# Kernel optimization log

Hardware: AMD Instinct MI355X
Metric: run time of the kernel (lower is better)

## Reference

```python
import jax, jax.numpy as jnp
import numpy as np

EPS = 1e-5


def mish(x):
    return x * jnp.tanh(jax.nn.softplus(x))


def layer_norm(x, g, b):
    mu = jnp.mean(x, axis=-1, keepdims=True)
    var = jnp.var(x, axis=-1, keepdims=True)
    return (x - mu) / jnp.sqrt(var + EPS) * g + b


def setup_inputs() -> dict:
    key = jax.random.key(0)
    ks = jax.random.split(key, 10)
    D = 256      # hidden_size == encoder feature dim
    L = 64       # max_length
    B, N, K, Q = 2, 10, 1, 5
    NQ = N * Q   # na_rate = 0
    s = 0.02
    inp = {
        "support": jax.random.normal(ks[0], (B * N * K, L, D), jnp.float32),
        "query": jax.random.normal(ks[1], (B * NQ, L, D), jnp.float32),
        "ln_g": jnp.ones((D,), jnp.float32),
        "ln_b": jnp.zeros((D,), jnp.float32),
        "ln2_g": jnp.ones((2 * D,), jnp.float32),
        "ln2_b": jnp.zeros((2 * D,), jnp.float32),
        "proj_W": jax.random.normal(ks[2], (D, 4 * D), jnp.float32) * s,
        "proj_b": jnp.zeros((D,), jnp.float32),
        "W1": jax.random.normal(ks[3], (D, 4 * D), jnp.float32) * s,
        "b1": jnp.zeros((D,), jnp.float32),
        "W2": jax.random.normal(ks[4], (1, D), jnp.float32) * s,
        "b2": jnp.zeros((1,), jnp.float32),
        "W3": jax.random.normal(ks[5], (1, 1), jnp.float32) * s,  # MLP_out Linear(K=1, 1)
        "b3": jnp.zeros((1,), jnp.float32),
        "N": N, "K": K, "Q": Q,
    }
    return inp


def reference(support, query, ln_g, ln_b, ln2_g, ln2_b, proj_W, proj_b,
              W1, b1, W2, b2, W3, b3, N, K, Q):
    L, D = support.shape[-2], support.shape[-1]
    B = support.shape[0] // (N * K)
    NQ = query.shape[0] // B  # = N*Q + na*Q

    s = layer_norm(support, ln_g, ln_b)
    q = layer_norm(query, ln_g, ln_b)

    # expand to all (query, support) pairs: [B, NQ, N*K, L, D] -> [M, L, D]
    s_e = jnp.broadcast_to(s.reshape(B, 1, N * K, L, D), (B, NQ, N * K, L, D)).reshape(-1, L, D)
    q_e = jnp.broadcast_to(q.reshape(B, NQ, 1, L, D), (B, NQ, N * K, L, D)).reshape(-1, L, D)

    # bidirectional cross-attention (no scaling, as in the original)
    att = jnp.einsum('mld,mkd->mlk', s_e, q_e)            # [M, Ls, Lq]
    s_att = jnp.einsum('mlk,mkd->mld', jax.nn.softmax(att, axis=2), q_e)
    q_att = jnp.einsum('mlk,mld->mkd', jax.nn.softmax(att, axis=1), s_e)

    enh_s = jnp.concatenate([s_e, s_att, jnp.abs(s_e - s_att), s_e * s_att], axis=-1)
    enh_q = jnp.concatenate([q_e, q_att, jnp.abs(q_e - q_att), q_e * q_att], axis=-1)
    s_p = mish(enh_s @ proj_W.T + proj_b)
    q_p = mish(enh_q @ proj_W.T + proj_b)

    # pool_norm: max+mean over length, then LayerNorm(2D)
    s_pool = layer_norm(jnp.concatenate([jnp.max(s_p, axis=-2), jnp.mean(s_p, axis=-2)], axis=-1), ln2_g, ln2_b)
    q_pool = layer_norm(jnp.concatenate([jnp.max(q_p, axis=-2), jnp.mean(q_p, axis=-2)], axis=-1), ln2_g, ln2_b)

    cat_seq = jnp.concatenate([q_pool, s_pool], axis=-1)  # [M, 4D]
    h = mish(cat_seq @ W1.T + b1) @ W2.T + b2             # MLProc -> [M, 1]
    logits = mish(h) @ W3.T + b3                          # MLP_out (K=1) -> [M, 1]

    logits = logits.reshape(B, NQ, N)
    minn = jnp.min(logits, axis=-1)
    logits = jnp.concatenate([logits, minn[..., None] - 1.0], axis=2)  # [B, NQ, N+1]
    pred = jnp.argmax(logits.reshape(-1, N + 1), axis=1)
    return logits, pred
```

## Files before the change

### kernel.cpp

```cpp
#include <hip/hip_runtime.h>

typedef unsigned int u32;
typedef unsigned short u16;
#define LN_EPS 1e-5f

typedef __attribute__((ext_vector_type(8))) short short8v;
typedef __attribute__((ext_vector_type(4))) float f32x4;

#define MFMA(acc, a, b) acc = __builtin_amdgcn_mfma_f32_16x16x32_bf16(a, b, acc, 0, 0, 0)

__device__ __forceinline__ float wave_sum(float v){
  #pragma unroll
  for (int o = 32; o > 0; o >>= 1) v += __shfl_xor(v, o, 64);
  return v;
}
__device__ __forceinline__ float mishf(float v){
  float t = __expf(v);
  float u = t*t + 2.f*t;
  return v * (1.f - 2.f/(u + 2.f));
}
__device__ __forceinline__ float bf2f(u16 h){
  return __uint_as_float(((u32)h) << 16);
}
__device__ __forceinline__ u32 pack_split(float x){
  u32 u = __float_as_uint(x);
  u32 h = (u + 0x8000u) & 0xffff0000u;
  float lf = x - __uint_as_float(h);
  return h | (__float_as_uint(lf) >> 16);
}
__device__ __forceinline__ void split_pair(float x0, float x1, u32& hw, u32& lw){
  u32 u0 = __float_as_uint(x0), u1 = __float_as_uint(x1);
  u32 h0 = (u0 + 0x8000u) & 0xffff0000u;
  u32 h1 = (u1 + 0x8000u) & 0xffff0000u;
  float l0 = x0 - __uint_as_float(h0);
  float l1 = x1 - __uint_as_float(h1);
  hw = (h0 >> 16) | h1;
  lw = (__float_as_uint(l0) >> 16) | (__float_as_uint(l1) & 0xffff0000u);
}
__device__ __forceinline__ void split8v(f32x4 a, f32x4 b, short8v& hi, short8v& lo){
  union { short8v v; u32 w[4]; } H, L;
  split_pair(a[0], a[1], H.w[0], L.w[0]);
  split_pair(a[2], a[3], H.w[1], L.w[1]);
  split_pair(b[0], b[1], H.w[2], L.w[2]);
  split_pair(b[2], b[3], H.w[3], L.w[3]);
  hi = H.v; lo = L.v;
}
__device__ __forceinline__ void unpack8(uint4 q0, uint4 q1, short8v& hi, short8v& lo){
  union { short8v v; u32 w[4]; } H, L;
  H.w[0] = (q0.x >> 16) | (q0.y & 0xffff0000u);
  L.w[0] = (q0.x & 0xffffu) | (q0.y << 16);
  H.w[1] = (q0.z >> 16) | (q0.w & 0xffff0000u);
  L.w[1] = (q0.z & 0xffffu) | (q0.w << 16);
  H.w[2] = (q1.x >> 16) | (q1.y & 0xffff0000u);
  L.w[2] = (q1.x & 0xffffu) | (q1.y << 16);
  H.w[3] = (q1.z >> 16) | (q1.w & 0xffff0000u);
  L.w[3] = (q1.z & 0xffffu) | (q1.w << 16);
  hi = H.v; lo = L.v;
}

__global__ void k_setup_A(const float* __restrict__ sup, const float* __restrict__ qry,
                          const float* __restrict__ lng, const float* __restrict__ lnb,
                          const float* __restrict__ Wg,  const float* __restrict__ W1,
                          u16* __restrict__ SHI, u16* __restrict__ SLO,
                          u16* __restrict__ QHI, u16* __restrict__ QLO,
                          u16* __restrict__ WHI, u16* __restrict__ WLO,
                          float* __restrict__ W1T2)
{
  const int bid = blockIdx.x, t = threadIdx.x;

  if (bid < 120){
    const int seq = bid;
    const float* src; u16 *dh, *dl;
    if (seq < 20){
      src = sup + (size_t)seq*16384;
      dh = SHI + (size_t)seq*16384; dl = SLO + (size_t)seq*16384;
    } else {
      src = qry + (size_t)(seq-20)*16384;
      dh = QHI + (size_t)(seq-20)*16384; dl = QLO + (size_t)(seq-20)*16384;
    }
    const int w = t >> 6, lane = t & 63;
    float4 g4 = *(const float4*)(lng + lane*4);
    float4 b4 = *(const float4*)(lnb + lane*4);
    for (int r = w; r < 64; r += 4){
      float4 x = *(const float4*)(src + r*256 + lane*4);
      float s  = wave_sum(x.x + x.y + x.z + x.w);
      float sq = wave_sum(x.x*x.x + x.y*x.y + x.z*x.z + x.w*x.w);
      float mu = s*(1.f/256.f);
      float rstd = 1.f/sqrtf(sq*(1.f/256.f) - mu*mu + LN_EPS);
      float y0 = (x.x - mu)*rstd*g4.x + b4.x;
      float y1 = (x.y - mu)*rstd*g4.y + b4.y;
      float y2 = (x.z - mu)*rstd*g4.z + b4.z;
      float y3 = (x.w - mu)*rstd*g4.w + b4.w;
      u32 p0 = pack_split(y0), p1 = pack_split(y1), p2 = pack_split(y2), p3 = pack_split(y3);
      ushort4 hv = make_ushort4((u16)(p0>>16),(u16)(p1>>16),(u16)(p2>>16),(u16)(p3>>16));
      ushort4 lv = make_ushort4((u16)(p0&0xffffu),(u16)(p1&0xffffu),(u16)(p2&0xffffu),(u16)(p3&0xffffu));
      *(ushort4*)(dh + r*256 + lane*4) = hv;
      *(ushort4*)(dl + r*256 + lane*4) = lv;
    }
  } else if (bid < 248){
    const int gid = (bid-120)*256 + t;
    const int ks = gid >> 10, rem = gid & 1023, nt = rem >> 6, l = rem & 63;
    const int n  = nt*16 + (l & 15);
    const int k0 = ks*32 + (l >> 4)*8;
    const float* src = Wg + n*1024 + k0;
    float4 xa = *(const float4*)src;
    float4 xb = *(const float4*)(src + 4);
    f32x4 fa, fb;
    fa[0]=xa.x; fa[1]=xa.y; fa[2]=xa.z; fa[3]=xa.w;
    fb[0]=xb.x; fb[1]=xb.y; fb[2]=xb.z; fb[3]=xb.w;
    short8v hi, lo;
    split8v(fa, fb, hi, lo);
    *(short8v*)(WHI + (size_t)gid*8) = hi;
    *(short8v*)(WLO + (size_t)gid*8) = lo;
  } else {
    const int gid = (bid-248)*256 + t;
    const int kb = gid >> 8, n = gid & 255;
    float4 v = *(const float4*)(W1 + n*1024 + kb*4);
    *(float4*)(W1T2 + kb*1024 + n*4) = v;
  }
}

__global__ __launch_bounds__(256) void k_setup_xp(
    const u16* __restrict__ SHI, const u16* __restrict__ SLO,
    const u16* __restrict__ QHI, const u16* __restrict__ QLO,
    const u16* __restrict__ WHI, const u16* __restrict__ WLO,
    float* __restrict__ XPS, float* __restrict__ XPQ)
{
  const int seq = blockIdx.x;
  const u16 *Xh, *Xl; float* out;
  if (seq < 20){
    Xh = SHI + (size_t)seq*16384; Xl = SLO + (size_t)seq*16384;
    out = XPS + (size_t)seq*16384;
  } else {
    Xh = QHI + (size_t)(seq-20)*16384; Xl = QLO + (size_t)(seq-20)*16384;
    out = XPQ + (size_t)(seq-20)*16384;
  }
  const int t = threadIdx.x, w = t >> 6, l = t & 63;
  const int l15 = l & 15, l4 = l >> 4;
  const int Mg = w >> 1, Ng = w & 1;

  f32x4 acc[2][8];
  #pragma unroll
  for (int i = 0; i < 2; i++)
    #pragma unroll
    for (int j = 0; j < 8; j++){ acc[i][j][0]=0.f; acc[i][j][1]=0.f; acc[i][j][2]=0.f; acc[i][j][3]=0.f; }

  for (int ks = 0; ks < 8; ks++){
    short8v ah[2], al[2];
    #pragma unroll
    for (int mt = 0; mt < 2; mt++){
      const int ro = (Mg*32 + mt*16 + l15)*256 + ks*32 + l4*8;
      ah[mt] = *(const short8v*)(Xh + ro);
      al[mt] = *(const short8v*)(Xl + ro);
    }
    #pragma unroll
    for (int nt = 0; nt < 8; nt++){
      const int fo = (ks*16 + Ng*8 + nt)*512 + l*8;
      short8v bh = *(const short8v*)(WHI + fo);
      short8v bl = *(const short8v*)(WLO + fo);
      #pragma unroll
      for (int mt = 0; mt < 2; mt++){
        MFMA(acc[mt][nt], ah[mt], bh);
        MFMA(acc[mt][nt], ah[mt], bl);
        MFMA(acc[mt][nt], al[mt], bh);
      }
    }
  }
  #pragma unroll
  for (int mt = 0; mt < 2; mt++)
    #pragma unroll
    for (int nt = 0; nt < 8; nt++)
      #pragma unroll
      for (int r = 0; r < 4; r++)
        out[(Mg*32 + mt*16 + l4*4 + r)*256 + Ng*128 + nt*16 + l15] = acc[mt][nt][r];
}

#define WLH(BUF, C, H) { const int base_ = (((C)*8 + ch)*16 + Ng*8 + (H)*4)*512 + l*8; \
  _Pragma("unroll") for (int j_ = 0; j_ < 4; j_++){ \
    BUF[j_*2]   = *(const short8v*)(WHI + base_ + j_*512); \
    BUF[j_*2+1] = *(const short8v*)(WLO + base_ + j_*512); } }
#define WMH(BUF, G, H) { _Pragma("unroll") for (int j_ = 0; j_ < 4; j_++){ \
  MFMA(acc[0][(H)*4+j_], fh[G][0], BUF[j_*2]); \
  MFMA(acc[0][(H)*4+j_], fh[G][0], BUF[j_*2+1]); \
  MFMA(acc[0][(H)*4+j_], fl[G][0], BUF[j_*2]); \
  MFMA(acc[1][(H)*4+j_], fh[G][1], BUF[j_*2]); \
  MFMA(acc[1][(H)*4+j_], fh[G][1], BUF[j_*2+1]); \
  MFMA(acc[1][(H)*4+j_], fl[G][1], BUF[j_*2]); } }

__global__ __launch_bounds__(256, 2) void k_pair15(
    const u16* __restrict__ SHI, const u16* __restrict__ SLO,
    const u16* __restrict__ QHI, const u16* __restrict__ QLO,
    const u16* __restrict__ WHI, const u16* __restrict__ WLO,
    const float* __restrict__ XPS, const float* __restrict__ XPQ,
    const float* __restrict__ W1T2,
    const float* __restrict__ pbias,
    const float* __restrict__ ln2g, const float* __restrict__ ln2b,
    const float* __restrict__ b1,
    const float* __restrict__ W2,  const float* __restrict__ b2,
    const float* __restrict__ W3,  const float* __restrict__ b3,
    float* __restrict__ logits)
{
  __shared__ float SM[19600];
  float* S0  = SM;
  u16*   OcT = (u16*)(SM + 4352);
  float* AOc = SM + 9472;
  u32*   P   = (u32*)(SM + 14080);
  float* cat = SM + 18432;
  float* smx = SM + 19456;
  float* smi = SM + 19520;
  float* red = SM + 19584;
  float* stat= SM + 19592;
  float* mred= SM + 19594;

  const int m = (blockIdx.x & 7)*125 + (blockIdx.x >> 3);
  const int b = m / 500, rr = m % 500, nq = rr / 10, n_ = rr % 10;
  const u16* Sh = SHI + (size_t)(b*10 + n_) * 16384;
  const u16* Sl = SLO + (size_t)(b*10 + n_) * 16384;
  const u16* Qh = QHI + (size_t)(b*50 + nq) * 16384;
  const u16* Ql = QLO + (size_t)(b*50 + nq) * 16384;
  const float* xpS = XPS + (size_t)(b*10 + n_) * 16384;
  const float* xpQ = XPQ + (size_t)(b*50 + nq) * 16384;

  const int t = threadIdx.x, w = t >> 6, l = t & 63;
  const int l15 = l & 15, l4 = l >> 4;

  {
    f32x4 acc4[4];
    #pragma unroll
    for (int i = 0; i < 4; i++){ acc4[i][0]=0.f; acc4[i][1]=0.f; acc4[i][2]=0.f; acc4[i][3]=0.f; }
    const u16* Sa = Sh + (w*16+l15)*256 + l4*8;
    const u16* Sb = Sl + (w*16+l15)*256 + l4*8;
    short8v ah = *(const short8v*)Sa;
    short8v al = *(const short8v*)Sb;
    short8v bh[4], bl[4];
    #pragma unroll
    for (int nt = 0; nt < 4; nt++){
      bh[nt] = *(const short8v*)(Qh + (nt*16+l15)*256 + l4*8);
      bl[nt] = *(const short8v*)(Ql + (nt*16+l15)*256 + l4*8);
    }
    #pragma unroll
    for (int ch = 0; ch < 8; ch++){
      short8v nah, nal, nbh[4], nbl[4];
      if (ch < 7){
        nah = *(const short8v*)(Sa + (ch+1)*32);
        nal = *(const short8v*)(Sb + (ch+1)*32);
        #pragma unroll
        for (int nt = 0; nt < 4; nt++){
          nbh[nt] = *(const short8v*)(Qh + (nt*16+l15)*256 + (ch+1)*32 + l4*8);
          nbl[nt] = *(const short8v*)(Ql + (nt*16+l15)*256 + (ch+1)*32 + l4*8);
        }
      }
      #pragma unroll
      for (int nt = 0; nt < 4; nt++){
        MFMA(acc4[nt], ah, bh[nt]);
        MFMA(acc4[nt], ah, bl[nt]);
        MFMA(acc4[nt], al, bh[nt]);
      }
      if (ch < 7){
        ah = nah; al = nal;
        #pragma unroll
        for (int nt = 0; nt < 4; nt++){ bh[nt] = nbh[nt]; bl[nt] = nbl[nt]; }
      }
    }
    #pragma unroll
    for (int nt = 0; nt < 4; nt++)
      #pragma unroll
      for (int r = 0; r < 4; r++)
        S0[(w*16 + l4*4 + r)*68 + nt*16 + l15] = acc4[nt][r];
    __syncthreads();
  }

  auto softmax_row = [&](){
    if (t < 64){
      float mxv = -1e30f, sm = 0.f;
      for (int k = 0; k < 64; k++) mxv = fmaxf(mxv, S0[t*68 + k]);
      for (int k = 0; k < 64; k++) sm += __expf(S0[t*68 + k] - mxv);
      smx[t] = mxv; smi[t] = 1.f/sm;
    }
    __syncthreads();
    #pragma unroll
    for (int r = 0; r < 16; r++){
      int idx = t + 256*r, ll = idx >> 6, k = idx & 63;
      P[ll*68 + k] = pack_split(__expf(S0[ll*68 + k] - smx[ll]) * smi[ll]);
    }
    __syncthreads();
  };
  auto softmax_col_T = [&](){
    if (t < 64){
      float mxv = -1e30f, sm = 0.f;
      for (int ld = 0; ld < 64; ld++) mxv = fmaxf(mxv, S0[ld*68 + t]);
      for (int ld = 0; ld < 64; ld++) sm += __expf(S0[ld*68 + t] - mxv);
      smx[t] = mxv; smi[t] = 1.f/sm;
    }
    __syncthreads();
    #pragma unroll
    for (int r = 0; r < 16; r++){
      int idx = t + 256*r, ll = idx >> 6, k = idx & 63;
      P[k*68 + ll] = pack_split(__expf(S0[ll*68 + k] - smx[k]) * smi[k]);
    }
    __syncthreads();
  };

  auto do_side = [&](const u16* Xh, const u16* Xl, const u16* Oh, const u16* Ol,
                     const float* xp, int cat_off){
    const int Mg = w >> 1, Ng = w & 1;
    f32x4 acc[2][8];
    #pragma unroll
    for (int mt = 0; mt < 2; mt++)
      #pragma unroll
      for (int nt = 0; nt < 8; nt++){
        const float* xr = xp + (Mg*32 + mt*16 + l4*4)*256 + Ng*128 + nt*16 + l15;
        acc[mt][nt][0] = xr[0];
        acc[mt][nt][1] = xr[256];
        acc[mt][nt][2] = xr[512];
        acc[mt][nt][3] = xr[768];
      }

    short8v svh = *(const short8v*)(Oh + l*256 + w*8);
    short8v svl = *(const short8v*)(Ol + l*256 + w*8);
    #pragma unroll
    for (int e = 0; e < 8; e++){
      OcT[(w*8+e)*80 + l]        = (u16)svh[e];
      OcT[2560 + (w*8+e)*80 + l] = (u16)svl[e];
    }
    svh = *(const short8v*)(Oh + l*256 + 32 + w*8);
    svl = *(const short8v*)(Ol + l*256 + 32 + w*8);
    __syncthreads();

    const int xoff = (Mg*32 + l15)*256 + l4*8;

    #pragma unroll 1
    for (int ch = 0; ch < 8; ch++){
      short8v xh0 = *(const short8v*)(Xh + xoff + ch*32);
      short8v xl0 = *(const short8v*)(Xl + xoff + ch*32);
      short8v xh1 = *(const short8v*)(Xh + xoff + 4096 + ch*32);
      short8v xl1 = *(const short8v*)(Xl + xoff + 4096 + ch*32);
      short8v wa[8], wb[8];
      WLH(wa, 1, 0);

      {
        const u16* Ob = OcT + (ch&1)*5120;
        f32x4 ao0 = {0.f,0.f,0.f,0.f}, ao1 = {0.f,0.f,0.f,0.f};
        #pragma unroll
        for (int ks = 0; ks < 2; ks++){
          const u32* pp = P + (w*16 + l15)*68 + ks*32 + l4*8;
          uint4 q0 = *(const uint4*)pp;
          uint4 q1 = *(const uint4*)(pp + 4);
          short8v ph, pl; unpack8(q0, q1, ph, pl);
          const u16* ob0 = Ob + l15*80 + ks*32 + l4*8;
          const u16* ob1 = Ob + (16 + l15)*80 + ks*32 + l4*8;
          short8v bh0 = *(const short8v*)ob0;
          short8v bl0 = *(const short8v*)(ob0 + 2560);
          short8v bh1 = *(const short8v*)ob1;
          short8v bl1 = *(const short8v*)(ob1 + 2560);
          MFMA(ao0, ph, bh0); MFMA(ao0, ph, bl0); MFMA(ao0, pl, bh0);
          MFMA(ao1, ph, bh1); MFMA(ao1, ph, bl1); MFMA(ao1, pl, bh1);
        }
        float* Ad = AOc + (ch&1)*2304;
        #pragma unroll
        for (int r = 0; r < 4; r++){
          Ad[(w*16 + l4*4 + r)*36 + l15]      = ao0[r];
          Ad[(w*16 + l4*4 + r)*36 + 16 + l15] = ao1[r];
        }
      }

      if (ch < 7){
        u16* Ob1 = OcT + ((ch+1)&1)*5120;
        #pragma unroll
        for (int e = 0; e < 8; e++){
          Ob1[(w*8+e)*80 + l]        = (u16)svh[e];
          Ob1[2560 + (w*8+e)*80 + l] = (u16)svl[e];
        }
      }
      if (ch < 6){
        svh = *(const short8v*)(Oh + l*256 + (ch+2)*32 + w*8);
        svl = *(const short8v*)(Ol + l*256 + (ch+2)*32 + w*8);
      }
      __syncthreads();

      short8v fh[3][2], fl[3][2];
      {
        const float* Ad = AOc + (ch&1)*2304;
        f32x4 xv0[2], xv1[2], av0[2], av1[2];
        #pragma unroll
        for (int mt_ = 0; mt_ < 2; mt_++){
          short8v xh = mt_ ? xh1 : xh0;
          short8v xl = mt_ ? xl1 : xl0;
          #pragma unroll
          for (int e_ = 0; e_ < 4; e_++){
            xv0[mt_][e_] = bf2f((u16)xh[e_])     + bf2f((u16)xl[e_]);
            xv1[mt_][e_] = bf2f((u16)xh[4 + e_]) + bf2f((u16)xl[4 + e_]);
          }
          const int row = Mg*32 + mt_*16 + l15;
          av0[mt_] = *(const f32x4*)(Ad + row*36 + l4*8);
          av1[mt_] = *(const f32x4*)(Ad + row*36 + l4*8 + 4);
        }
        #pragma unroll
        for (int mt_ = 0; mt_ < 2; mt_++){
          split8v(av0[mt_], av1[mt_], fh[0][mt_], fl[0][mt_]);
          f32x4 d0, d1, p0, p1;
          #pragma unroll
          for (int e_ = 0; e_ < 4; e_++){
            d0[e_] = fabsf(xv0[mt_][e_] - av0[mt_][e_]);
            d1[e_] = fabsf(xv1[mt_][e_] - av1[mt_][e_]);
            p0[e_] = xv0[mt_][e_] * av0[mt_][e_];
            p1[e_] = xv1[mt_][e_] * av1[mt_][e_];
          }
          split8v(d0, d1, fh[1][mt_], fl[1][mt_]);
          split8v(p0, p1, fh[2][mt_], fl[2][mt_]);
        }
      }

      WLH(wb, 1, 1);
      WMH(wa, 0, 0);
      WLH(wa, 2, 0);
      WMH(wb, 0, 1);
      WLH(wb, 2, 1);
      WMH(wa, 1, 0);
      WLH(wa, 3, 0);
      WMH(wb, 1, 1);
      WLH(wb, 3, 1);
      WMH(wa, 2, 0);
      WMH(wb, 2, 1);
    }

    float* pmax2 = (float*)P;
    float* psum2 = pmax2 + 512;
    #pragma unroll
    for (int nt = 0; nt < 8; nt++){
      const int col = Ng*128 + nt*16 + l15;
      const float pb = pbias[col];
      float mx = -1e30f, sm = 0.f;
      #pragma unroll
      for (int mt_ = 0; mt_ < 2; mt_++)
        #pragma unroll
        for (int r = 0; r < 4; r++){
          float v = mishf(acc[mt_][nt][r] + pb);
          mx = fmaxf(mx, v); sm += v;
        }
      mx = fmaxf(mx, __shfl_xor(mx, 16, 64));
      mx = fmaxf(mx, __shfl_xor(mx, 32, 64));
      sm += __shfl_xor(sm, 16, 64);
      sm += __shfl_xor(sm, 32, 64);
      if (l4 == 0){ pmax2[Mg*256 + col] = mx; psum2[Mg*256 + col] = sm; }
    }
    __syncthreads();
    float v1 = fmaxf(pmax2[t], pmax2[256 + t]);
    float v2 = (psum2[t] + psum2[256 + t]) * (1.f/64.f);
    float p1 = wave_sum(v1 + v2);
    float p2 = wave_sum(v1*v1 + v2*v2);
    if (l == 0){ red[w] = p1; red[4 + w] = p2; }
    __syncthreads();
    if (t == 0){
      float s1 = red[0]+red[1]+red[2]+red[3];
      float s2 = red[4]+red[5]+red[6]+red[7];
      float mu  = s1 * (1.f/512.f);
      float var = s2 * (1.f/512.f) - mu*mu;
      stat[0] = mu; stat[1] = 1.f/sqrtf(var + LN_EPS);
    }
    __syncthreads();
    float mu = stat[0], rstd = stat[1];
    cat[cat_off + t]       = (v1 - mu)*rstd*ln2g[t]       + ln2b[t];
    cat[cat_off + 256 + t] = (v2 - mu)*rstd*ln2g[256 + t] + ln2b[256 + t];
    __syncthreads();
  };

  softmax_row();
  do_side(Sh, Sl, Qh, Ql, xpS, 512);
  softmax_col_T();
  do_side(Qh, Ql, Sh, Sl, xpQ, 0);

  {
    float acc1 = 0.f;
    const float* wt = W1T2 + t*4;
    #pragma unroll 8
    for (int kb = 0; kb < 256; kb++){
      float4 wv = *(const float4*)(wt + kb*1024);
      const float* cp = &cat[kb*4];
      acc1 += cp[0]*wv.x + cp[1]*wv.y + cp[2]*wv.z + cp[3]*wv.w;
    }
    float hv = mishf(acc1 + b1[t]);
    float contrib = wave_sum(hv * W2[t]);
    if (l == 0) mred[w] = contrib;
  }
  __syncthreads();
  if (t == 0){
    float hh = mred[0] + mred[1] + mred[2] + mred[3] + b2[0];
    logits[m] = mishf(hh)*W3[0] + b3[0];
  }
}

__global__ void k_final9(const float* __restrict__ logits, float* __restrict__ out){
  int t = threadIdx.x;
  if (t < 100){
    float v[10];
    float mn = 1e30f;
    #pragma unroll
    for (int j = 0; j < 10; j++){ v[j] = logits[t*10 + j]; mn = fminf(mn, v[j]); }
    float best = -1e30f; int bi = 0;
    #pragma unroll
    for (int j = 0; j < 10; j++){ if (v[j] > best){ best = v[j]; bi = j; } }
    #pragma unroll
    for (int j = 0; j < 10; j++) out[t*11 + j] = v[j];
    out[t*11 + 10] = mn - 1.f;
    out[1100 + t] = (float)bi;
  }
}

extern "C" void kernel_launch(void* const* d_in, const int* in_sizes, int n_in,
                              void* d_out, int out_size, void* d_ws, size_t ws_size,
                              hipStream_t stream){
  (void)in_sizes; (void)n_in; (void)out_size; (void)ws_size;
  const float* support = (const float*)d_in[0];
  const float* query   = (const float*)d_in[1];
  const float* ln_g    = (const float*)d_in[2];
  const float* ln_b    = (const float*)d_in[3];
  const float* ln2_g   = (const float*)d_in[4];
  const float* ln2_b   = (const float*)d_in[5];
  const float* proj_W  = (const float*)d_in[6];
  const float* proj_b  = (const float*)d_in[7];
  const float* W1      = (const float*)d_in[8];
  const float* b1      = (const float*)d_in[9];
  const float* W2      = (const float*)d_in[10];
  const float* b2      = (const float*)d_in[11];
  const float* W3      = (const float*)d_in[12];
  const float* b3      = (const float*)d_in[13];

  char* wsb = (char*)d_ws;
  float* logits = (float*)wsb;
  u16* SHI = (u16*)(wsb + 4096);
  u16* SLO = SHI + (size_t)20*16384;
  u16* QHI = SLO + (size_t)20*16384;
  u16* QLO = QHI + (size_t)100*16384;
  u16* WHI = QLO + (size_t)100*16384;
  u16* WLO = WHI + (size_t)262144;
  float* XPS  = (float*)(WLO + (size_t)262144);
  float* XPQ  = XPS + (size_t)20*16384;
  float* W1T2 = XPQ + (size_t)100*16384;

  k_setup_A<<<dim3(504), dim3(256), 0, stream>>>(support, query, ln_g, ln_b,
                                                 proj_W, W1,
                                                 SHI, SLO, QHI, QLO, WHI, WLO,
                                                 W1T2);
  k_setup_xp<<<dim3(120), dim3(256), 0, stream>>>(SHI, SLO, QHI, QLO, WHI, WLO,
                                                  XPS, XPQ);
  k_pair15<<<dim3(1000), dim3(256), 0, stream>>>(SHI, SLO, QHI, QLO, WHI, WLO,
                                                 XPS, XPQ, W1T2,
                                                 proj_b, ln2_g, ln2_b,
                                                 b1, W2, b2, W3, b3, logits);
  k_final9<<<dim3(1), dim3(128), 0, stream>>>(logits, (float*)d_out);
}
```

Baseline: 395.5 us.

## Precompute support-side projection of query attention term via reassociation

For the query side, q_att·W_att is rewritten as P^T·(S·W_att) by associativity. S·W_att is precomputed per support sequence in the setup kernel and stored as split-bf16 MFMA fragments, so the pair kernel replaces a 64x256x256 chunk of its K loop with a 64x64x256 product. The setup kernel now converts proj_W fragments on the fly from fp32, and the pair kernel reads W1 directly instead of a transposed copy. Reassociation changes rounding order, and the extra hi/lo product adds MFMA work on the small GEMM.

```diff
diff --git a/kernel.cpp b/kernel.cpp
--- a/kernel.cpp
+++ b/kernel.cpp
@@ -60,11 +60,10 @@
 
 __global__ void k_setup_A(const float* __restrict__ sup, const float* __restrict__ qry,
                           const float* __restrict__ lng, const float* __restrict__ lnb,
-                          const float* __restrict__ Wg,  const float* __restrict__ W1,
+                          const float* __restrict__ Wg,
                           u16* __restrict__ SHI, u16* __restrict__ SLO,
                           u16* __restrict__ QHI, u16* __restrict__ QLO,
-                          u16* __restrict__ WHI, u16* __restrict__ WLO,
-                          float* __restrict__ W1T2)
+                          u16* __restrict__ WHI, u16* __restrict__ WLO)
 {
   const int bid = blockIdx.x, t = threadIdx.x;
 
@@ -97,11 +96,11 @@
       *(ushort4*)(dh + r*256 + lane*4) = hv;
       *(ushort4*)(dl + r*256 + lane*4) = lv;
     }
-  } else if (bid < 248){
+  } else {
     const int gid = (bid-120)*256 + t;
-    const int ks = gid >> 10, rem = gid & 1023, nt = rem >> 6, l = rem & 63;
+    const int ksb = gid >> 10, rem = gid & 1023, nt = rem >> 6, l = rem & 63;
     const int n  = nt*16 + (l & 15);
-    const int k0 = ks*32 + (l >> 4)*8;
+    const int k0 = (ksb + 8)*32 + (l >> 4)*8;
     const float* src = Wg + n*1024 + k0;
     float4 xa = *(const float4*)src;
     float4 xb = *(const float4*)(src + 4);
@@ -112,70 +111,96 @@
     split8v(fa, fb, hi, lo);
     *(short8v*)(WHI + (size_t)gid*8) = hi;
     *(short8v*)(WLO + (size_t)gid*8) = lo;
-  } else {
-    const int gid = (bid-248)*256 + t;
-    const int kb = gid >> 8, n = gid & 255;
-    float4 v = *(const float4*)(W1 + n*1024 + kb*4);
-    *(float4*)(W1T2 + kb*1024 + n*4) = v;
   }
 }
 
 __global__ __launch_bounds__(256) void k_setup_xp(
     const u16* __restrict__ SHI, const u16* __restrict__ SLO,
     const u16* __restrict__ QHI, const u16* __restrict__ QLO,
-    const u16* __restrict__ WHI, const u16* __restrict__ WLO,
-    float* __restrict__ XPS, float* __restrict__ XPQ)
+    const float* __restrict__ Wg,
+    float* __restrict__ XPS, float* __restrict__ XPQ,
+    u16* __restrict__ OWFH_S, u16* __restrict__ OWFL_S)
 {
   const int seq = blockIdx.x;
-  const u16 *Xh, *Xl; float* out;
+  const u16 *Xh, *Xl; float* outp;
   if (seq < 20){
     Xh = SHI + (size_t)seq*16384; Xl = SLO + (size_t)seq*16384;
-    out = XPS + (size_t)seq*16384;
+    outp = XPS + (size_t)seq*16384;
   } else {
     Xh = QHI + (size_t)(seq-20)*16384; Xl = QLO + (size_t)(seq-20)*16384;
-    out = XPQ + (size_t)(seq-20)*16384;
+    outp = XPQ + (size_t)(seq-20)*16384;
   }
   const int t = threadIdx.x, w = t >> 6, l = t & 63;
   const int l15 = l & 15, l4 = l >> 4;
   const int Mg = w >> 1, Ng = w & 1;
 
-  f32x4 acc[2][8];
-  #pragma unroll
-  for (int i = 0; i < 2; i++)
-    #pragma unroll
-    for (int j = 0; j < 8; j++){ acc[i][j][0]=0.f; acc[i][j][1]=0.f; acc[i][j][2]=0.f; acc[i][j][3]=0.f; }
-
-  for (int ks = 0; ks < 8; ks++){
-    short8v ah[2], al[2];
-    #pragma unroll
-    for (int mt = 0; mt < 2; mt++){
-      const int ro = (Mg*32 + mt*16 + l15)*256 + ks*32 + l4*8;
-      ah[mt] = *(const short8v*)(Xh + ro);
-      al[mt] = *(const short8v*)(Xl + ro);
-    }
-    #pragma unroll
-    for (int nt = 0; nt < 8; nt++){
-      const int fo = (ks*16 + Ng*8 + nt)*512 + l*8;
-      short8v bh = *(const short8v*)(WHI + fo);
-      short8v bl = *(const short8v*)(WLO + fo);
+  auto wfrag = [&](int kstep, int ntile, short8v& bh, short8v& bl){
+    const float* src = Wg + (ntile*16 + l15)*1024 + kstep*32 + l4*8;
+    float4 xa = *(const float4*)src;
+    float4 xb = *(const float4*)(src + 4);
+    f32x4 fa, fb;
+    fa[0]=xa.x; fa[1]=xa.y; fa[2]=xa.z; fa[3]=xa.w;
+    fb[0]=xb.x; fb[1]=xb.y; fb[2]=xb.z; fb[3]=xb.w;
+    split8v(fa, fb, bh, bl);
+  };
+
+  for (int c = 0; c < 2; c++){
+    if (c == 1 && seq >= 20) break;
+    f32x4 acc[2][8];
+    #pragma unroll
+    for (int i = 0; i < 2; i++)
+      #pragma unroll
+      for (int j = 0; j < 8; j++){ acc[i][j][0]=0.f; acc[i][j][1]=0.f; acc[i][j][2]=0.f; acc[i][j][3]=0.f; }
+
+    for (int ks = 0; ks < 8; ks++){
+      short8v ah[2], al[2];
       #pragma unroll
       for (int mt = 0; mt < 2; mt++){
-        MFMA(acc[mt][nt], ah[mt], bh);
-        MFMA(acc[mt][nt], ah[mt], bl);
-        MFMA(acc[mt][nt], al[mt], bh);
+        const int ro = (Mg*32 + mt*16 + l15)*256 + ks*32 + l4*8;
+        ah[mt] = *(const short8v*)(Xh + ro);
+        al[mt] = *(const short8v*)(Xl + ro);
+      }
+      #pragma unroll
+      for (int nt = 0; nt < 8; nt++){
+        short8v bh, bl;
+        wfrag(c*8 + ks, Ng*8 + nt, bh, bl);
+        #pragma unroll
+        for (int mt = 0; mt < 2; mt++){
+          MFMA(acc[mt][nt], ah[mt], bh);
+          MFMA(acc[mt][nt], ah[mt], bl);
+          MFMA(acc[mt][nt], al[mt], bh);
+        }
+      }
+    }
+    if (c == 0){
+      #pragma unroll
+      for (int mt = 0; mt < 2; mt++)
+        #pragma unroll
+        for (int nt = 0; nt < 8; nt++)
+          #pragma unroll
+          for (int r = 0; r < 4; r++)
+            outp[(Mg*32 + mt*16 + l4*4 + r)*256 + Ng*128 + nt*16 + l15] = acc[mt][nt][r];
+    } else {
+      u16* ofh = OWFH_S + (size_t)seq*16384;
+      u16* ofl = OWFL_S + (size_t)seq*16384;
+      #pragma unroll
+      for (int mt = 0; mt < 2; mt++){
+        const int lane_f = (2*mt + (l4 >> 1))*16 + l15;
+        #pragma unroll
+        for (int nt = 0; nt < 8; nt++){
+          u32 h0, l0, h1, l1;
+          split_pair(acc[mt][nt][0], acc[mt][nt][1], h0, l0);
+          split_pair(acc[mt][nt][2], acc[mt][nt][3], h1, l1);
+          const int off = ((Mg*16 + Ng*8 + nt)*64 + lane_f)*8 + (l4 & 1)*4;
+          *(ushort4*)(ofh + off) = make_ushort4((u16)h0, (u16)(h0>>16), (u16)h1, (u16)(h1>>16));
+          *(ushort4*)(ofl + off) = make_ushort4((u16)l0, (u16)(l0>>16), (u16)l1, (u16)(l1>>16));
+        }
       }
     }
   }
-  #pragma unroll
-  for (int mt = 0; mt < 2; mt++)
-    #pragma unroll
-    for (int nt = 0; nt < 8; nt++)
-      #pragma unroll
-      for (int r = 0; r < 4; r++)
-        out[(Mg*32 + mt*16 + l4*4 + r)*256 + Ng*128 + nt*16 + l15] = acc[mt][nt][r];
-}
-
-#define WLH(BUF, C, H) { const int base_ = (((C)*8 + ch)*16 + Ng*8 + (H)*4)*512 + l*8; \
+}
+
+#define WLH(BUF, C, H) { const int base_ = (((((C)-1))*8 + ch)*16 + Ng*8 + (H)*4)*512 + l*8; \
   _Pragma("unroll") for (int j_ = 0; j_ < 4; j_++){ \
     BUF[j_*2]   = *(const short8v*)(WHI + base_ + j_*512); \
     BUF[j_*2+1] = *(const short8v*)(WLO + base_ + j_*512); } }
@@ -187,15 +212,15 @@
   MFMA(acc[1][(H)*4+j_], fh[G][1], BUF[j_*2+1]); \
   MFMA(acc[1][(H)*4+j_], fl[G][1], BUF[j_*2]); } }
 
-__global__ __launch_bounds__(256, 2) void k_pair15(
+__global__ __launch_bounds__(256, 2) void k_pair17(
     const u16* __restrict__ SHI, const u16* __restrict__ SLO,
     const u16* __restrict__ QHI, const u16* __restrict__ QLO,
     const u16* __restrict__ WHI, const u16* __restrict__ WLO,
     const float* __restrict__ XPS, const float* __restrict__ XPQ,
-    const float* __restrict__ W1T2,
+    const u16* __restrict__ OWFH_S, const u16* __restrict__ OWFL_S,
     const float* __restrict__ pbias,
     const float* __restrict__ ln2g, const float* __restrict__ ln2b,
-    const float* __restrict__ b1,
+    const float* __restrict__ W1,  const float* __restrict__ b1,
     const float* __restrict__ W2,  const float* __restrict__ b2,
     const float* __restrict__ W3,  const float* __restrict__ b3,
     float* __restrict__ logits)
@@ -220,6 +245,8 @@
   const u16* Ql = QLO + (size_t)(b*50 + nq) * 16384;
   const float* xpS = XPS + (size_t)(b*10 + n_) * 16384;
   const float* xpQ = XPQ + (size_t)(b*50 + nq) * 16384;
+  const u16* owhS = OWFH_S + (size_t)(b*10 + n_) * 16384;
+  const u16* owlS = OWFL_S + (size_t)(b*10 + n_) * 16384;
 
   const int t = threadIdx.x, w = t >> 6, l = t & 63;
   const int l15 = l & 15, l4 = l >> 4;
@@ -301,8 +328,50 @@
     __syncthreads();
   };
 
-  auto do_side = [&](const u16* Xh, const u16* Xl, const u16* Oh, const u16* Ol,
-                     const float* xp, int cat_off){
+  auto pool_ln2 = [&](f32x4 (&acc)[2][8], int Mg, int Ng, int cat_off){
+    float* pmax2 = (float*)P;
+    float* psum2 = pmax2 + 512;
+    #pragma unroll
+    for (int nt = 0; nt < 8; nt++){
+      const int col = Ng*128 + nt*16 + l15;
+      const float pb = pbias[col];
+      float mx = -1e30f, sm = 0.f;
+      #pragma unroll
+      for (int mt_ = 0; mt_ < 2; mt_++)
+        #pragma unroll
+        for (int r = 0; r < 4; r++){
+          float v = mishf(acc[mt_][nt][r] + pb);
+          mx = fmaxf(mx, v); sm += v;
+        }
+      mx = fmaxf(mx, __shfl_xor(mx, 16, 64));
+      mx = fmaxf(mx, __shfl_xor(mx, 32, 64));
+      sm += __shfl_xor(sm, 16, 64);
+      sm += __shfl_xor(sm, 32, 64);
+      if (l4 == 0){ pmax2[Mg*256 + col] = mx; psum2[Mg*256 + col] = sm; }
+    }
+    __syncthreads();
+    float v1 = fmaxf(pmax2[t], pmax2[256 + t]);
+    float v2 = (psum2[t] + psum2[256 + t]) * (1.f/64.f);
+    float p1 = wave_sum(v1 + v2);
+    float p2 = wave_sum(v1*v1 + v2*v2);
+    if (l == 0){ red[w] = p1; red[4 + w] = p2; }
+    __syncthreads();
+    if (t == 0){
+      float s1 = red[0]+red[1]+red[2]+red[3];
+      float s2 = red[4]+red[5]+red[6]+red[7];
+      float mu  = s1 * (1.f/512.f);
+      float var = s2 * (1.f/512.f) - mu*mu;
+      stat[0] = mu; stat[1] = 1.f/sqrtf(var + LN_EPS);
+    }
+    __syncthreads();
+    float mu = stat[0], rstd = stat[1];
+    cat[cat_off + t]       = (v1 - mu)*rstd*ln2g[t]       + ln2b[t];
+    cat[cat_off + 256 + t] = (v2 - mu)*rstd*ln2g[256 + t] + ln2b[256 + t];
+    __syncthreads();
+  };
+
+  auto do_sideS = [&](const u16* Xh, const u16* Xl, const u16* Oh, const u16* Ol,
+                      const float* xp, int cat_off){
     const int Mg = w >> 1, Ng = w & 1;
     f32x4 acc[2][8];
     #pragma unroll
@@ -423,61 +492,168 @@
       WMH(wa, 2, 0);
       WMH(wb, 2, 1);
     }
-
-    float* pmax2 = (float*)P;
-    float* psum2 = pmax2 + 512;
-    #pragma unroll
-    for (int nt = 0; nt < 8; nt++){
-      const int col = Ng*128 + nt*16 + l15;
-      const float pb = pbias[col];
-      float mx = -1e30f, sm = 0.f;
-      #pragma unroll
-      for (int mt_ = 0; mt_ < 2; mt_++)
+    pool_ln2(acc, Mg, Ng, cat_off);
+  };
+
+  auto do_sideQ = [&](const u16* Xh, const u16* Xl, const u16* Oh, const u16* Ol,
+                      const float* xp, const u16* Owh, const u16* Owl, int cat_off){
+    const int Mg = w >> 1, Ng = w & 1;
+    f32x4 acc[2][8];
+    #pragma unroll
+    for (int mt = 0; mt < 2; mt++)
+      #pragma unroll
+      for (int nt = 0; nt < 8; nt++){
+        const float* xr = xp + (Mg*32 + mt*16 + l4*4)*256 + Ng*128 + nt*16 + l15;
+        acc[mt][nt][0] = xr[0];
+        acc[mt][nt][1] = xr[256];
+        acc[mt][nt][2] = xr[512];
+        acc[mt][nt][3] = xr[768];
+      }
+
+    short8v svh = *(const short8v*)(Oh + l*256 + w*8);
+    short8v svl = *(const short8v*)(Ol + l*256 + w*8);
+
+    #pragma unroll
+    for (int ks = 0; ks < 2; ks++){
+      short8v ph[2], pl[2];
+      #pragma unroll
+      for (int mt = 0; mt < 2; mt++){
+        const u32* pp = P + (Mg*32 + mt*16 + l15)*68 + ks*32 + l4*8;
+        uint4 q0 = *(const uint4*)pp;
+        uint4 q1 = *(const uint4*)(pp + 4);
+        unpack8(q0, q1, ph[mt], pl[mt]);
+      }
+      #pragma unroll
+      for (int nt = 0; nt < 8; nt++){
+        const int fo = ((ks*16 + Ng*8 + nt)*64 + l)*8;
+        short8v bh = *(const short8v*)(Owh + fo);
+        short8v bl = *(const short8v*)(Owl + fo);
+        #pragma unroll
+        for (int mt = 0; mt < 2; mt++){
+          MFMA(acc[mt][nt], ph[mt], bh);
+          MFMA(acc[mt][nt], ph[mt], bl);
+          MFMA(acc[mt][nt], pl[mt], bh);
+          MFMA(acc[mt][nt], pl[mt], bl);
+        }
+      }
+    }
+
+    #pragma unroll
+    for (int e = 0; e < 8; e++){
+      OcT[(w*8+e)*80 + l]        = (u16)svh[e];
+      OcT[2560 + (w*8+e)*80 + l] = (u16)svl[e];
+    }
+    svh = *(const short8v*)(Oh + l*256 + 32 + w*8);
+    svl = *(const short8v*)(Ol + l*256 + 32 + w*8);
+    __syncthreads();
+
+    const int xoff = (Mg*32 + l15)*256 + l4*8;
+
+    #pragma unroll 1
+    for (int ch = 0; ch < 8; ch++){
+      short8v xh0 = *(const short8v*)(Xh + xoff + ch*32);
+      short8v xl0 = *(const short8v*)(Xl + xoff + ch*32);
+      short8v xh1 = *(const short8v*)(Xh + xoff + 4096 + ch*32);
+      short8v xl1 = *(const short8v*)(Xl + xoff + 4096 + ch*32);
+      short8v wa[8], wb[8];
+      WLH(wa, 2, 0);
+
+      {
+        const u16* Ob = OcT + (ch&1)*5120;
+        f32x4 ao0 = {0.f,0.f,0.f,0.f}, ao1 = {0.f,0.f,0.f,0.f};
+        #pragma unroll
+        for (int ks = 0; ks < 2; ks++){
+          const u32* pp = P + (w*16 + l15)*68 + ks*32 + l4*8;
+          uint4 q0 = *(const uint4*)pp;
+          uint4 q1 = *(const uint4*)(pp + 4);
+          short8v ph, pl; unpack8(q0, q1, ph, pl);
+          const u16* ob0 = Ob + l15*80 + ks*32 + l4*8;
+          const u16* ob1 = Ob + (16 + l15)*80 + ks*32 + l4*8;
+          short8v bh0 = *(const short8v*)ob0;
+          short8v bl0 = *(const short8v*)(ob0 + 2560);
+          short8v bh1 = *(const short8v*)ob1;
+          short8v bl1 = *(const short8v*)(ob1 + 2560);
+          MFMA(ao0, ph, bh0); MFMA(ao0, ph, bl0); MFMA(ao0, pl, bh0);
+          MFMA(ao1, ph, bh1); MFMA(ao1, ph, bl1); MFMA(ao1, pl, bh1);
+        }
+        float* Ad = AOc + (ch&1)*2304;
         #pragma unroll
         for (int r = 0; r < 4; r++){
-          float v = mishf(acc[mt_][nt][r] + pb);
-          mx = fmaxf(mx, v); sm += v;
-        }
-      mx = fmaxf(mx, __shfl_xor(mx, 16, 64));
-      mx = fmaxf(mx, __shfl_xor(mx, 32, 64));
-      sm += __shfl_xor(sm, 16, 64);
-      sm += __shfl_xor(sm, 32, 64);
-      if (l4 == 0){ pmax2[Mg*256 + col] = mx; psum2[Mg*256 + col] = sm; }
-    }
-    __syncthreads();
-    float v1 = fmaxf(pmax2[t], pmax2[256 + t]);
-    float v2 = (psum2[t] + psum2[256 + t]) * (1.f/64.f);
-    float p1 = wave_sum(v1 + v2);
-    float p2 = wave_sum(v1*v1 + v2*v2);
-    if (l == 0){ red[w] = p1; red[4 + w] = p2; }
-    __syncthreads();
-    if (t == 0){
-      float s1 = red[0]+red[1]+red[2]+red[3];
-      float s2 = red[4]+red[5]+red[6]+red[7];
-      float mu  = s1 * (1.f/512.f);
-      float var = s2 * (1.f/512.f) - mu*mu;
-      stat[0] = mu; stat[1] = 1.f/sqrtf(var + LN_EPS);
-    }
-    __syncthreads();
-    float mu = stat[0], rstd = stat[1];
-    cat[cat_off + t]       = (v1 - mu)*rstd*ln2g[t]       + ln2b[t];
-    cat[cat_off + 256 + t] = (v2 - mu)*rstd*ln2g[256 + t] + ln2b[256 + t];
-    __syncthreads();
+          Ad[(w*16 + l4*4 + r)*36 + l15]      = ao0[r];
+          Ad[(w*16 + l4*4 + r)*36 + 16 + l15] = ao1[r];
+        }
+      }
+
+      if (ch < 7){
+        u16* Ob1 = OcT + ((ch+1)&1)*5120;
+        #pragma unroll
+        for (int e = 0; e < 8; e++){
+          Ob1[(w*8+e)*80 + l]        = (u16)svh[e];
+          Ob1[2560 + (w*8+e)*80 + l] = (u16)svl[e];
+        }
+      }
+      if (ch < 6){
+        svh = *(const short8v*)(Oh + l*256 + (ch+2)*32 + w*8);
+        svl = *(const short8v*)(Ol + l*256 + (ch+2)*32 + w*8);
+      }
+      __syncthreads();
+
+      short8v fh[2][2], fl[2][2];
+      {
+        const float* Ad = AOc + (ch&1)*2304;
+        f32x4 xv0[2], xv1[2], av0[2], av1[2];
+        #pragma unroll
+        for (int mt_ = 0; mt_ < 2; mt_++){
+          short8v xh = mt_ ? xh1 : xh0;
+          short8v xl = mt_ ? xl1 : xl0;
+          #pragma unroll
+          for (int e_ = 0; e_ < 4; e_++){
+            xv0[mt_][e_] = bf2f((u16)xh[e_])     + bf2f((u16)xl[e_]);
+            xv1[mt_][e_] = bf2f((u16)xh[4 + e_]) + bf2f((u16)xl[4 + e_]);
+          }
+          const int row = Mg*32 + mt_*16 + l15;
+          av0[mt_] = *(const f32x4*)(Ad + row*36 + l4*8);
+          av1[mt_] = *(const f32x4*)(Ad + row*36 + l4*8 + 4);
+        }
+        #pragma unroll
+        for (int mt_ = 0; mt_ < 2; mt_++){
+          f32x4 d0, d1, p0, p1;
+          #pragma unroll
+          for (int e_ = 0; e_ < 4; e_++){
+            d0[e_] = fabsf(xv0[mt_][e_] - av0[mt_][e_]);
+            d1[e_] = fabsf(xv1[mt_][e_] - av1[mt_][e_]);
+            p0[e_] = xv0[mt_][e_] * av0[mt_][e_];
+            p1[e_] = xv1[mt_][e_] * av1[mt_][e_];
+          }
+          split8v(d0, d1, fh[0][mt_], fl[0][mt_]);
+          split8v(p0, p1, fh[1][mt_], fl[1][mt_]);
+        }
+      }
+
+      WLH(wb, 2, 1);
+      WMH(wa, 0, 0);
+      WLH(wa, 3, 0);
+      WMH(wb, 0, 1);
+      WLH(wb, 3, 1);
+      WMH(wa, 1, 0);
+      WMH(wb, 1, 1);
+    }
+    pool_ln2(acc, Mg, Ng, cat_off);
   };
 
   softmax_row();
-  do_side(Sh, Sl, Qh, Ql, xpS, 512);
+  do_sideS(Sh, Sl, Qh, Ql, xpS, 512);
   softmax_col_T();
-  do_side(Qh, Ql, Sh, Sl, xpQ, 0);
+  do_sideQ(Qh, Ql, Sh, Sl, xpQ, owhS, owlS, 0);
 
   {
+    const float* wr = W1 + t*1024;
     float acc1 = 0.f;
-    const float* wt = W1T2 + t*4;
-    #pragma unroll 8
-    for (int kb = 0; kb < 256; kb++){
-      float4 wv = *(const float4*)(wt + kb*1024);
-      const float* cp = &cat[kb*4];
-      acc1 += cp[0]*wv.x + cp[1]*wv.y + cp[2]*wv.z + cp[3]*wv.w;
+    #pragma unroll 4
+    for (int i = 0; i < 256; i++){
+      float4 u4 = *(const float4*)(wr + i*4);
+      const float* cp = &cat[i*4];
+      acc1 += cp[0]*u4.x + cp[1]*u4.y + cp[2]*u4.z + cp[3]*u4.w;
     }
     float hv = mishf(acc1 + b1[t]);
     float contrib = wave_sum(hv * W2[t]);
@@ -533,20 +709,20 @@
   u16* QHI = SLO + (size_t)20*16384;
   u16* QLO = QHI + (size_t)100*16384;
   u16* WHI = QLO + (size_t)100*16384;
-  u16* WLO = WHI + (size_t)262144;
-  float* XPS  = (float*)(WLO + (size_t)262144);
+  u16* WLO = WHI + (size_t)196608;
+  float* XPS  = (float*)(WLO + (size_t)196608);
   float* XPQ  = XPS + (size_t)20*16384;
-  float* W1T2 = XPQ + (size_t)100*16384;
-
-  k_setup_A<<<dim3(504), dim3(256), 0, stream>>>(support, query, ln_g, ln_b,
-                                                 proj_W, W1,
-                                                 SHI, SLO, QHI, QLO, WHI, WLO,
-                                                 W1T2);
-  k_setup_xp<<<dim3(120), dim3(256), 0, stream>>>(SHI, SLO, QHI, QLO, WHI, WLO,
-                                                  XPS, XPQ);
-  k_pair15<<<dim3(1000), dim3(256), 0, stream>>>(SHI, SLO, QHI, QLO, WHI, WLO,
-                                                 XPS, XPQ, W1T2,
+  u16* OWFH_S = (u16*)(XPQ + (size_t)100*16384);
+  u16* OWFL_S = OWFH_S + (size_t)20*16384;
+
+  k_setup_A<<<dim3(216), dim3(256), 0, stream>>>(support, query, ln_g, ln_b,
+                                                 proj_W,
+                                                 SHI, SLO, QHI, QLO, WHI, WLO);
+  k_setup_xp<<<dim3(120), dim3(256), 0, stream>>>(SHI, SLO, QHI, QLO, proj_W,
+                                                  XPS, XPQ, OWFH_S, OWFL_S);
+  k_pair17<<<dim3(1000), dim3(256), 0, stream>>>(SHI, SLO, QHI, QLO, WHI, WLO,
+                                                 XPS, XPQ, OWFH_S, OWFL_S,
                                                  proj_b, ln2_g, ln2_b,
-                                                 b1, W2, b2, W3, b3, logits);
+                                                 W1, b1, W2, b2, W3, b3, logits);
   k_final9<<<dim3(1), dim3(128), 0, stream>>>(logits, (float*)d_out);
 }
```

Result: slower. 500.3 us (+26.5%).

## Shrink LDS and registers in pair kernel to fit three blocks per CU

Applied to the files above, without the earlier changes.

Shared memory drops from about 78KB to 52KB. The attention score buffer S0 now aliases OcT, so the score matrix is recomputed before the column softmax instead of being kept. AOc loses its double buffer and an extra barrier is added per chunk. Weight prefetch buffers are halved (4 instead of 8 short8v), and launch bounds rise to 3 blocks per CU, trading extra attention MFMAs and synchronisation for higher occupancy.

```diff
diff --git a/kernel.cpp b/kernel.cpp
--- a/kernel.cpp
+++ b/kernel.cpp
@@ -175,19 +175,18 @@
         out[(Mg*32 + mt*16 + l4*4 + r)*256 + Ng*128 + nt*16 + l15] = acc[mt][nt][r];
 }
 
-#define WLH(BUF, C, H) { const int base_ = (((C)*8 + ch)*16 + Ng*8 + (H)*4)*512 + l*8; \
-  _Pragma("unroll") for (int j_ = 0; j_ < 4; j_++){ \
-    BUF[j_*2]   = *(const short8v*)(WHI + base_ + j_*512); \
-    BUF[j_*2+1] = *(const short8v*)(WLO + base_ + j_*512); } }
-#define WMH(BUF, G, H) { _Pragma("unroll") for (int j_ = 0; j_ < 4; j_++){ \
-  MFMA(acc[0][(H)*4+j_], fh[G][0], BUF[j_*2]); \
-  MFMA(acc[0][(H)*4+j_], fh[G][0], BUF[j_*2+1]); \
-  MFMA(acc[0][(H)*4+j_], fl[G][0], BUF[j_*2]); \
-  MFMA(acc[1][(H)*4+j_], fh[G][1], BUF[j_*2]); \
-  MFMA(acc[1][(H)*4+j_], fh[G][1], BUF[j_*2+1]); \
-  MFMA(acc[1][(H)*4+j_], fl[G][1], BUF[j_*2]); } }
-
-__global__ __launch_bounds__(256, 2) void k_pair15(
+#define WL2(BUF, C, S) { const int base_ = (((C)*8 + ch)*16 + Ng*8 + (S)*2)*512 + l*8; \
+  BUF[0] = *(const short8v*)(WHI + base_); \
+  BUF[1] = *(const short8v*)(WLO + base_); \
+  BUF[2] = *(const short8v*)(WHI + base_ + 512); \
+  BUF[3] = *(const short8v*)(WLO + base_ + 512); }
+#define WM2(BUF, G, S) { \
+  MFMA(acc[0][(S)*2],   fh[G][0], BUF[0]); MFMA(acc[0][(S)*2],   fh[G][0], BUF[1]); MFMA(acc[0][(S)*2],   fl[G][0], BUF[0]); \
+  MFMA(acc[1][(S)*2],   fh[G][1], BUF[0]); MFMA(acc[1][(S)*2],   fh[G][1], BUF[1]); MFMA(acc[1][(S)*2],   fl[G][1], BUF[0]); \
+  MFMA(acc[0][(S)*2+1], fh[G][0], BUF[2]); MFMA(acc[0][(S)*2+1], fh[G][0], BUF[3]); MFMA(acc[0][(S)*2+1], fl[G][0], BUF[2]); \
+  MFMA(acc[1][(S)*2+1], fh[G][1], BUF[2]); MFMA(acc[1][(S)*2+1], fh[G][1], BUF[3]); MFMA(acc[1][(S)*2+1], fl[G][1], BUF[2]); }
+
+__global__ __launch_bounds__(256, 3) void k_pair18(
     const u16* __restrict__ SHI, const u16* __restrict__ SLO,
     const u16* __restrict__ QHI, const u16* __restrict__ QLO,
     const u16* __restrict__ WHI, const u16* __restrict__ WLO,
@@ -200,17 +199,17 @@
     const float* __restrict__ W3,  const float* __restrict__ b3,
     float* __restrict__ logits)
 {
-  __shared__ float SM[19600];
+  __shared__ float SM[12944];
   float* S0  = SM;
-  u16*   OcT = (u16*)(SM + 4352);
-  float* AOc = SM + 9472;
-  u32*   P   = (u32*)(SM + 14080);
-  float* cat = SM + 18432;
-  float* smx = SM + 19456;
-  float* smi = SM + 19520;
-  float* red = SM + 19584;
-  float* stat= SM + 19592;
-  float* mred= SM + 19594;
+  u16*   OcT = (u16*)SM;
+  float* AOc = SM + 5120;
+  u32*   P   = (u32*)(SM + 7424);
+  float* cat = SM + 11776;
+  float* smx = SM + 12800;
+  float* smi = SM + 12864;
+  float* red = SM + 12928;
+  float* stat= SM + 12936;
+  float* mred= SM + 12938;
 
   const int m = (blockIdx.x & 7)*125 + (blockIdx.x >> 3);
   const int b = m / 500, rr = m % 500, nq = rr / 10, n_ = rr % 10;
@@ -224,7 +223,7 @@
   const int t = threadIdx.x, w = t >> 6, l = t & 63;
   const int l15 = l & 15, l4 = l >> 4;
 
-  {
+  auto compute_att = [&](){
     f32x4 acc4[4];
     #pragma unroll
     for (int i = 0; i < 4; i++){ acc4[i][0]=0.f; acc4[i][1]=0.f; acc4[i][2]=0.f; acc4[i][3]=0.f; }
@@ -268,7 +267,7 @@
       for (int r = 0; r < 4; r++)
         S0[(w*16 + l4*4 + r)*68 + nt*16 + l15] = acc4[nt][r];
     __syncthreads();
-  }
+  };
 
   auto softmax_row = [&](){
     if (t < 64){
@@ -335,8 +334,8 @@
       short8v xl0 = *(const short8v*)(Xl + xoff + ch*32);
       short8v xh1 = *(const short8v*)(Xh + xoff + 4096 + ch*32);
       short8v xl1 = *(const short8v*)(Xl + xoff + 4096 + ch*32);
-      short8v wa[8], wb[8];
-      WLH(wa, 1, 0);
+      short8v wa[4], wb[4];
+      WL2(wa, 1, 0);
 
       {
         const u16* Ob = OcT + (ch&1)*5120;
@@ -356,13 +355,13 @@
           MFMA(ao0, ph, bh0); MFMA(ao0, ph, bl0); MFMA(ao0, pl, bh0);
           MFMA(ao1, ph, bh1); MFMA(ao1, ph, bl1); MFMA(ao1, pl, bh1);
         }
-        float* Ad = AOc + (ch&1)*2304;
         #pragma unroll
         for (int r = 0; r < 4; r++){
-          Ad[(w*16 + l4*4 + r)*36 + l15]      = ao0[r];
-          Ad[(w*16 + l4*4 + r)*36 + 16 + l15] = ao1[r];
-        }
-      }
+          AOc[(w*16 + l4*4 + r)*36 + l15]      = ao0[r];
+          AOc[(w*16 + l4*4 + r)*36 + 16 + l15] = ao1[r];
+        }
+      }
+      __syncthreads();
 
       if (ch < 7){
         u16* Ob1 = OcT + ((ch+1)&1)*5120;
@@ -376,11 +375,9 @@
         svh = *(const short8v*)(Oh + l*256 + (ch+2)*32 + w*8);
         svl = *(const short8v*)(Ol + l*256 + (ch+2)*32 + w*8);
       }
-      __syncthreads();
 
       short8v fh[3][2], fl[3][2];
       {
-        const float* Ad = AOc + (ch&1)*2304;
         f32x4 xv0[2], xv1[2], av0[2], av1[2];
         #pragma unroll
         for (int mt_ = 0; mt_ < 2; mt_++){
@@ -392,8 +389,8 @@
             xv1[mt_][e_] = bf2f((u16)xh[4 + e_]) + bf2f((u16)xl[4 + e_]);
           }
           const int row = Mg*32 + mt_*16 + l15;
-          av0[mt_] = *(const f32x4*)(Ad + row*36 + l4*8);
-          av1[mt_] = *(const f32x4*)(Ad + row*36 + l4*8 + 4);
+          av0[mt_] = *(const f32x4*)(AOc + row*36 + l4*8);
+          av1[mt_] = *(const f32x4*)(AOc + row*36 + l4*8 + 4);
         }
         #pragma unroll
         for (int mt_ = 0; mt_ < 2; mt_++){
@@ -411,17 +408,19 @@
         }
       }
 
-      WLH(wb, 1, 1);
-      WMH(wa, 0, 0);
-      WLH(wa, 2, 0);
-      WMH(wb, 0, 1);
-      WLH(wb, 2, 1);
-      WMH(wa, 1, 0);
-      WLH(wa, 3, 0);
-      WMH(wb, 1, 1);
-      WLH(wb, 3, 1);
-      WMH(wa, 2, 0);
-      WMH(wb, 2, 1);
+      WL2(wb, 1, 1); WM2(wa, 0, 0);
+      WL2(wa, 1, 2); WM2(wb, 0, 1);
+      WL2(wb, 1, 3); WM2(wa, 0, 2);
+      WL2(wa, 2, 0); WM2(wb, 0, 3);
+      WL2(wb, 2, 1); WM2(wa, 1, 0);
+      WL2(wa, 2, 2); WM2(wb, 1, 1);
+      WL2(wb, 2, 3); WM2(wa, 1, 2);
+      WL2(wa, 3, 0); WM2(wb, 1, 3);
+      WL2(wb, 3, 1); WM2(wa, 2, 0);
+      WL2(wa, 3, 2); WM2(wb, 2, 1);
+      WL2(wb, 3, 3); WM2(wa, 2, 2);
+                     WM2(wb, 2, 3);
+      __syncthreads();
     }
 
     float* pmax2 = (float*)P;
@@ -465,8 +464,10 @@
     __syncthreads();
   };
 
+  compute_att();
   softmax_row();
   do_side(Sh, Sl, Qh, Ql, xpS, 512);
+  compute_att();
   softmax_col_T();
   do_side(Qh, Ql, Sh, Sl, xpQ, 0);
 
@@ -544,7 +545,7 @@
                                                  W1T2);
   k_setup_xp<<<dim3(120), dim3(256), 0, stream>>>(SHI, SLO, QHI, QLO, WHI, WLO,
                                                   XPS, XPQ);
-  k_pair15<<<dim3(1000), dim3(256), 0, stream>>>(SHI, SLO, QHI, QLO, WHI, WLO,
+  k_pair18<<<dim3(1000), dim3(256), 0, stream>>>(SHI, SLO, QHI, QLO, WHI, WLO,
                                                  XPS, XPQ, W1T2,
                                                  proj_b, ln2_g, ln2_b,
                                                  b1, W2, b2, W3, b3, logits);
```

Result: slower. 649.6 us (+64.2%).
